# Optimization experiments

Measured on AMD Instinct MI355X. Metric: run time of the kernel, lower is better.

Reference implementation:

```python
import jax, jax.numpy as jnp
import numpy as np

B, S, D, L, V = 2, 1024, 1024, 8, 32000
EPS = 1e-8


def rmsnorm(x, w):
    return x * jax.lax.rsqrt(jnp.mean(x * x, axis=-1, keepdims=True) + EPS) * w


def lerp_scan(v, a):
    # h_t = (1 - a_t) * h_{t-1} + a_t * v_t over time axis=1 (h_0 = 0)
    A = 1.0 - a
    Bv = a * v
    def comb(l, r):
        return (l[0] * r[0], l[1] * r[0] + r[1])
    _, h = jax.lax.associative_scan(comb, (A, Bv), axis=1)
    return h


def mrt_layer(x, kw, cw, cb, w1, b1, w2, b2, nw):
    res = x @ kw                                   # [B,S,2D]
    theta, alpha = jnp.split(res, 2, axis=-1)
    h = lerp_scan(jnp.tanh(theta) * jnp.pi, jax.nn.sigmoid(alpha))  # [B,S,D]
    # causal depthwise conv, kernel 3, manual left pad of 2
    hc = jnp.pad(h.transpose(0, 2, 1), ((0, 0), (0, 0), (2, 0)))    # [B,D,S+2]
    hb = jax.lax.conv_general_dilated(
        hc, cw, window_strides=(1,), padding='VALID',
        dimension_numbers=('NCH', 'OIH', 'NCH'), feature_group_count=D)
    hb = (hb + cb[None, :, None]).transpose(0, 2, 1)                # [B,S,D]
    z = h + hb
    hf = jax.nn.silu(z @ w1 + b1) @ w2 + b2
    return rmsnorm(hf, nw)


def setup_inputs() -> dict:
    key = jax.random.key(0)
    ks = jax.random.split(key, 10)
    s = 0.02
    return {
        'input_ids': jax.random.randint(ks[0], (B, S), 0, V),
        'embedding': jax.random.normal(ks[1], (V, D), dtype=jnp.float32) * 0.002,
        'pos_emb': jax.random.normal(ks[2], (1, 1024, D), dtype=jnp.float32) * 0.002,
        'keygen_w': jax.random.normal(ks[3], (L, D, 2 * D), dtype=jnp.float32) * s,
        'conv_w': jax.random.normal(ks[4], (L, D, 1, 3), dtype=jnp.float32) * s,
        'conv_b': jnp.zeros((L, D), dtype=jnp.float32),
        'mlp_w1': jax.random.normal(ks[5], (L, D, 2 * D), dtype=jnp.float32) * s,
        'mlp_b1': jnp.zeros((L, 2 * D), dtype=jnp.float32),
        'mlp_w2': jax.random.normal(ks[6], (L, 2 * D, D), dtype=jnp.float32) * s,
        'mlp_b2': jnp.zeros((L, D), dtype=jnp.float32),
        'norm_w': jnp.ones((L, D), dtype=jnp.float32),
        'plastic': jnp.zeros((4, D, D), dtype=jnp.float32),
        'final_norm_w': jnp.ones((D,), dtype=jnp.float32),
    }


def reference(input_ids, embedding, pos_emb, keygen_w, conv_w, conv_b,
              mlp_w1, mlp_b1, mlp_w2, mlp_b2, norm_w, plastic, final_norm_w):
    seq = input_ids.shape[1]
    x = embedding[input_ids] + pos_emb[:, :seq, :]
    x = x / jnp.maximum(jnp.linalg.norm(x, axis=-1, keepdims=True), 1e-12)  # F.normalize
    for i in range(L):
        delta = mrt_layer(x, keygen_w[i], conv_w[i], conv_b[i],
                          mlp_w1[i], mlp_b1[i], mlp_w2[i], mlp_b2[i], norm_w[i])
        if i >= L - 4:
            x = x + delta + delta @ plastic[i - (L - 4)]
        else:
            x = x + delta
    x = rmsnorm(x, final_norm_w)
    # eval mode: dropout is identity
    x = x * jax.lax.rsqrt(jnp.mean(x * x, axis=-1, keepdims=True) + 1e-8) * 0.8
    logits = x @ embedding.T                       # tied lm_head
    std = jnp.std(logits, axis=-1, keepdims=True, ddof=1)  # torch.std unbiased
    logits = logits / jnp.maximum(std, 1.0)
    return jnp.clip(logits, -10.0, 10.0)
```

## Files before the change

kernel.cpp:

```cpp
#include <hip/hip_runtime.h>


using short8 = __attribute__((ext_vector_type(8))) short;
using half8  = __attribute__((ext_vector_type(8))) _Float16;
using f32x4  = __attribute__((ext_vector_type(4))) float;

#define DEVI __device__ __forceinline__

DEVI float sigm(float x) { return 1.0f / (1.0f + expf(-x)); }

DEVI float block_sum256(float v) {
  #pragma unroll
  for (int o = 32; o > 0; o >>= 1) v += __shfl_down(v, o, 64);
  __shared__ float sm[4];
  if ((threadIdx.x & 63) == 0) sm[threadIdx.x >> 6] = v;
  __syncthreads();
  float t = sm[0] + sm[1] + sm[2] + sm[3];
  __syncthreads();
  return t;
}

DEVI void gload16(const void* g, void* l) {
  __builtin_amdgcn_global_load_lds(
      (const __attribute__((address_space(1))) unsigned*)g,
      (__attribute__((address_space(3))) unsigned*)l, 16, 0, 0);
}

template<int EPI, int KSPLIT>
__global__ __launch_bounds__(256, 2) void gemm9(
    const _Float16* __restrict__ A, const _Float16* __restrict__ B,
    int M, int N, int K,
    float* __restrict__ outF, _Float16* __restrict__ outH,
    const float* __restrict__ bias,
    float* __restrict__ psum, float* __restrict__ psq, int halfN)
{
  __shared__ __align__(16) unsigned short lds[2][2][128 * 64];
  const int tid  = threadIdx.x;
  const int lane = tid & 63, wid = tid >> 6;
  const int wr = wid >> 1, wc = wid & 1;
  const int myr = lane & 15;
  const int kq  = lane >> 4;

  const int nwg  = gridDim.x;
  const int flat = blockIdx.x;
  const int swz  = (flat & 7) * (nwg >> 3) + (flat >> 3);
  const int ks   = (KSPLIT > 1) ? (swz % KSPLIT) : 0;
  const int tile = (KSPLIT > 1) ? (swz / KSPLIT) : swz;
  const int MT   = M >> 7;
  const int m0   = (tile % MT) * 128;
  const int nt   = tile / MT;
  const int n0   = nt * 128;
  const int Kc   = K / KSPLIT;
  const int kbase = ks * Kc;
  const int NT   = Kc / 64;

  auto stage = [&](int b, int k0) {
    #pragma unroll
    for (int q = 0; q < 4; ++q) {
      const int row  = q * 32 + wid * 8 + (lane >> 3);
      const int scol = ((lane & 7) ^ (row & 7)) << 3;
      const int lb   = (q * 32 + wid * 8) * 64;
      gload16(A + (size_t)(m0 + row) * K + k0 + scol, &lds[b][0][lb]);
      gload16(B + (size_t)(n0 + row) * K + k0 + scol, &lds[b][1][lb]);
    }
  };

  f32x4 acc[4][4] = {};

  stage(0, kbase);
  stage(1, kbase + 64);
  for (int t = 0; t < NT; ++t) {
    const int b = t & 1;
    if (t + 1 < NT) { asm volatile("s_waitcnt vmcnt(8)" ::: "memory"); }
    else            { asm volatile("s_waitcnt vmcnt(0)" ::: "memory"); }
    __builtin_amdgcn_s_barrier();
    asm volatile("" ::: "memory");

    #pragma unroll
    for (int kk = 0; kk < 2; ++kk) {
      short8 af[4], bf[4];
      #pragma unroll
      for (int i = 0; i < 4; ++i) {
        const int ra = wr * 64 + i * 16 + myr;
        af[i] = *(const short8*)&lds[b][0][ra * 64 + (((kk * 4 + kq) ^ (ra & 7)) << 3)];
      }
      #pragma unroll
      for (int j = 0; j < 4; ++j) {
        const int rb = wc * 64 + j * 16 + myr;
        bf[j] = *(const short8*)&lds[b][1][rb * 64 + (((kk * 4 + kq) ^ (rb & 7)) << 3)];
      }
      asm volatile("s_waitcnt lgkmcnt(0)" ::: "memory");
      if (kk == 1) {
        __builtin_amdgcn_s_barrier();
        asm volatile("" ::: "memory");
        if (t + 2 < NT) stage(b, kbase + (t + 2) * 64);
      }
      __builtin_amdgcn_sched_barrier(0);
      __builtin_amdgcn_s_setprio(1);
      #pragma unroll
      for (int i = 0; i < 4; ++i)
        #pragma unroll
        for (int j = 0; j < 4; ++j)
          acc[i][j] = __builtin_amdgcn_mfma_f32_16x16x32_f16(
              __builtin_bit_cast(half8, af[i]), __builtin_bit_cast(half8, bf[j]),
              acc[i][j], 0, 0, 0);
      __builtin_amdgcn_s_setprio(0);
    }
  }

  const size_t MN = (size_t)M * N;
  #pragma unroll
  for (int i = 0; i < 4; ++i) {
    const int rbase = m0 + wr * 64 + i * 16 + (kq << 2);
    #pragma unroll
    for (int j = 0; j < 4; ++j) {
      const int col = n0 + wc * 64 + j * 16 + myr;
      if constexpr (EPI == 1) {
        f32x4 v;
        #pragma unroll
        for (int r = 0; r < 4; ++r) {
          float c = acc[i][j][r];
          v[r] = (col < halfN) ? (tanhf(c) * 3.14159265358979323846f) : sigm(c);
        }
        *(f32x4*)&outF[(size_t)col * M + rbase] = v;
      } else {
        #pragma unroll
        for (int r = 0; r < 4; ++r) {
          float c = acc[i][j][r];
          const size_t idx = (size_t)(rbase + r) * N + col;
          if constexpr (EPI == 0) {
            outF[idx] = c;
          } else if constexpr (EPI == 2) {
            c += bias[col];
            outH[idx] = (_Float16)(c * sigm(c));
          } else if constexpr (EPI == 4) {
            float xn = outF[idx] + c;
            outF[idx] = xn;
            outH[idx] = (_Float16)xn;
          } else if constexpr (EPI == 5) {
            outF[(size_t)ks * MN + idx] = c;
          }
        }
      }
    }
  }

  if constexpr (EPI == 0) {
    const int PW = N >> 6;
    const int pcol = nt * 2 + wc;
    #pragma unroll
    for (int i = 0; i < 4; ++i)
      #pragma unroll
      for (int r = 0; r < 4; ++r) {
        float s = 0.f, ss = 0.f;
        #pragma unroll
        for (int j = 0; j < 4; ++j) {
          float v = acc[i][j][r];
          s += v; ss += v * v;
        }
        #pragma unroll
        for (int mk = 1; mk < 16; mk <<= 1) {
          s  += __shfl_xor(s,  mk, 64);
          ss += __shfl_xor(ss, mk, 64);
        }
        if (myr == i * 4 + r) {
          const int row = m0 + wr * 64 + i * 16 + kq * 4 + r;
          psum[(size_t)row * PW + pcol] = s;
          psq [(size_t)row * PW + pcol] = ss;
        }
      }
  }
}

__global__ __launch_bounds__(256) void scanconv(
    const float* __restrict__ vaT, const float* __restrict__ cw,
    const float* __restrict__ cb, _Float16* __restrict__ z16,
    int S, int D, int M)
{
  const int dl = threadIdx.x & 7;
  const int c  = threadIdx.x >> 3;
  const int ch = blockIdx.x * 8 + dl;
  const int b = ch >> 10, d = ch & 1023;
  const float* vrow = vaT + (size_t)d * M + b * S;
  const float* arow = vaT + (size_t)(D + d) * M + b * S;
  const int s0 = c * 32;

  f32x4 vr[8], ar[8];
  float A = 1.f, Bv = 0.f, Apm = 1.f, Bpm = 0.f;
  #pragma unroll
  for (int t = 0; t < 8; ++t) {
    vr[t] = *(const f32x4*)&vrow[s0 + t * 4];
    ar[t] = *(const f32x4*)&arow[s0 + t * 4];
    #pragma unroll
    for (int r = 0; r < 4; ++r) {
      if (t * 4 + r == 31) { Apm = A; Bpm = Bv; }
      float na = 1.f - ar[t][r];
      A *= na;
      Bv = Bv * na + ar[t][r] * vr[t][r];
    }
  }
  __shared__ float Asm[32][9], Bsm[32][9], Aps[32][9], Bps[32][9];
  Asm[c][dl] = A; Bsm[c][dl] = Bv; Aps[c][dl] = Apm; Bps[c][dl] = Bpm;
  __syncthreads();
  if (threadIdx.x < 8) {
    float run = 0.f;
    for (int cc = 0; cc < 32; ++cc) {
      float A_ = Asm[cc][dl], B_ = Bsm[cc][dl];
      Bsm[cc][dl] = run;
      run = A_ * run + B_;
    }
  }
  __syncthreads();
  float hm1 = Bsm[c][dl];
  float hm2 = (c == 0) ? 0.f
            : (Aps[c - 1][dl] * Bsm[c - 1][dl] + Bps[c - 1][dl]);

  const float w0 = cw[d * 3 + 0], w1 = cw[d * 3 + 1], w2 = cw[d * 3 + 2];
  const float bc = cb[d];
  #pragma unroll
  for (int t = 0; t < 8; ++t) {
    #pragma unroll
    for (int r = 0; r < 4; ++r) {
      float h = hm1 + ar[t][r] * (vr[t][r] - hm1);
      float z = h + bc + w0 * hm2 + w1 * hm1 + w2 * h;
      z16[(size_t)(b * S + s0 + t * 4 + r) * D + d] = (_Float16)z;
      hm2 = hm1; hm1 = h;
    }
  }
}

__global__ __launch_bounds__(256) void rms_fuse(
    const float* __restrict__ p, const float* __restrict__ bias,
    const float* __restrict__ nw, float* __restrict__ x,
    _Float16* __restrict__ o16, int D, int mode, size_t MN)
{
  const size_t base = (size_t)blockIdx.x * D;
  float vloc[4]; float ss = 0.f;
  #pragma unroll
  for (int q = 0; q < 4; ++q) {
    int d = threadIdx.x + q * 256;
    float v = p[base + d] + p[MN + base + d] + bias[d];
    vloc[q] = v; ss += v * v;
  }
  ss = block_sum256(ss);
  float r = 1.f / sqrtf(ss / D + 1e-8f);
  #pragma unroll
  for (int q = 0; q < 4; ++q) {
    int d = threadIdx.x + q * 256;
    float delta = vloc[q] * r * nw[d];
    float xn = x[base + d] + delta;
    x[base + d] = xn;
    o16[base + d] = (_Float16)(mode ? delta : xn);
  }
}

__global__ __launch_bounds__(256) void embed_norm(
    const int* __restrict__ ids, const float* __restrict__ emb,
    const float* __restrict__ pos,
    float* __restrict__ x, _Float16* __restrict__ x16, int S, int D)
{
  const int rowi = blockIdx.x;
  const int s = rowi % S;
  const int tok = ids[rowi];
  const size_t eb = (size_t)tok * D, pb = (size_t)s * D, xb = (size_t)rowi * D;
  float vloc[4]; float ss = 0.f;
  #pragma unroll
  for (int q = 0; q < 4; ++q) {
    int d = threadIdx.x + q * 256;
    float v = emb[eb + d] + pos[pb + d];
    vloc[q] = v; ss += v * v;
  }
  ss = block_sum256(ss);
  float r = 1.f / fmaxf(sqrtf(ss), 1e-12f);
  #pragma unroll
  for (int q = 0; q < 4; ++q) {
    int d = threadIdx.x + q * 256;
    float v = vloc[q] * r;
    x[xb + d] = v;
    x16[xb + d] = (_Float16)v;
  }
}

__global__ __launch_bounds__(256) void final_norm(
    const float* __restrict__ x, const float* __restrict__ w,
    _Float16* __restrict__ xf, int D)
{
  const size_t base = (size_t)blockIdx.x * D;
  float s1 = 0.f, s2 = 0.f;
  float vloc[4], wloc[4];
  #pragma unroll
  for (int q = 0; q < 4; ++q) {
    int d = threadIdx.x + q * 256;
    float v = x[base + d], ww = w[d];
    vloc[q] = v; wloc[q] = ww;
    s1 += v * v; s2 += v * ww * v * ww;
  }
  s1 = block_sum256(s1);
  s2 = block_sum256(s2);
  float r1 = 1.f / sqrtf(s1 / D + 1e-8f);
  float m2 = r1 * r1 * (s2 / D);
  float r2 = 1.f / sqrtf(m2 + 1e-8f);
  float sc = r1 * r2 * 0.8f;
  #pragma unroll
  for (int q = 0; q < 4; ++q) {
    int d = threadIdx.x + q * 256;
    xf[base + d] = (_Float16)(vloc[q] * wloc[q] * sc);
  }
}

__global__ __launch_bounds__(256) void fix_row(
    float* __restrict__ out, const float* __restrict__ psum,
    const float* __restrict__ psq, int PW, int V)
{
  const int row = blockIdx.x;
  float s = 0.f, q = 0.f;
  for (int j = threadIdx.x; j < PW; j += 256) {
    s += psum[(size_t)row * PW + j];
    q += psq [(size_t)row * PW + j];
  }
  s = block_sum256(s);
  q = block_sum256(q);
  float mean = s / V;
  float var = (q - (float)V * mean * mean) / (float)(V - 1);
  var = fmaxf(var, 0.f);
  const float sc = 1.f / fmaxf(sqrtf(var), 1.f);
  float* rowp = out + (size_t)row * V;
  for (int j = threadIdx.x * 4; j < V; j += 1024) {
    f32x4 v = *(f32x4*)&rowp[j];
    #pragma unroll
    for (int t = 0; t < 4; ++t)
      v[t] = fminf(fmaxf(v[t] * sc, -10.f), 10.f);
    *(f32x4*)&rowp[j] = v;
  }
}

__global__ void tsplit16(const float* __restrict__ W, _Float16* __restrict__ WT,
                         int K, int N)
{
  __shared__ float t[32][33];
  const size_t bo = (size_t)blockIdx.z * K * N;
  const int tx = threadIdx.x, ty = threadIdx.y;
  #pragma unroll
  for (int i = 0; i < 32; i += 8) {
    int kk = blockIdx.y * 32 + ty + i;
    int nn = blockIdx.x * 32 + tx;
    t[ty + i][tx] = W[bo + (size_t)kk * N + nn];
  }
  __syncthreads();
  #pragma unroll
  for (int i = 0; i < 32; i += 8) {
    int nn = blockIdx.x * 32 + ty + i;
    int kk = blockIdx.y * 32 + tx;
    WT[bo + (size_t)nn * K + kk] = (_Float16)t[tx][ty + i];
  }
}

__global__ void cvt_f16(const float* __restrict__ in, _Float16* __restrict__ o, size_t n)
{
  for (size_t i = (size_t)blockIdx.x * 256 + threadIdx.x; i < n;
       i += (size_t)gridDim.x * 256)
    o[i] = (_Float16)in[i];
}

extern "C" void kernel_launch(void* const* d_in, const int* in_sizes, int n_in,
                              void* d_out, int out_size, void* d_ws, size_t ws_size,
                              hipStream_t stream)
{
  (void)in_sizes; (void)n_in; (void)out_size; (void)ws_size;
  const int*   ids = (const int*)  d_in[0];
  const float* emb = (const float*)d_in[1];
  const float* pos = (const float*)d_in[2];
  const float* kw  = (const float*)d_in[3];
  const float* cw  = (const float*)d_in[4];
  const float* cb  = (const float*)d_in[5];
  const float* w1  = (const float*)d_in[6];
  const float* b1  = (const float*)d_in[7];
  const float* w2  = (const float*)d_in[8];
  const float* b2  = (const float*)d_in[9];
  const float* nw  = (const float*)d_in[10];
  const float* pl  = (const float*)d_in[11];
  const float* fnw = (const float*)d_in[12];
  float* out = (float*)d_out;

  constexpr int B = 2, S = 1024, D = 1024, L = 8, V = 32000;
  constexpr int M = B * S;
  const size_t MN = (size_t)M * D;

  size_t off = 0;
  auto alloc = [&](size_t bytes) {
    char* p = (char*)d_ws + off;
    off += (bytes + 255) & ~(size_t)255;
    return (void*)p;
  };
  _Float16* kwT  = (_Float16*)alloc((size_t)L * 2 * D * D * 2);
  _Float16* w1T  = (_Float16*)alloc((size_t)L * 2 * D * D * 2);
  _Float16* w2T  = (_Float16*)alloc((size_t)L * 2 * D * D * 2);
  _Float16* plT  = (_Float16*)alloc((size_t)4 * D * D * 2);
  _Float16* emb16 = (_Float16*)alloc((size_t)V * D * 2);
  float* x    = (float*)alloc(MN * 4);
  _Float16* x16 = (_Float16*)alloc(MN * 2);
  float* vaT  = (float*)alloc((size_t)M * 2 * D * 4);
  float* pbig = (float*)alloc(2 * MN * 4);
  _Float16* z16 = (_Float16*)alloc(MN * 2);
  _Float16* u16 = (_Float16*)alloc((size_t)M * 2 * D * 2);
  _Float16* d16 = (_Float16*)alloc(MN * 2);
  _Float16* xf16 = (_Float16*)alloc(MN * 2);

  const int PW = V >> 6;
  float* psum = vaT;
  float* psq  = vaT + (size_t)M * PW;

  {
    dim3 tb(32, 8);
    tsplit16<<<dim3(2 * D / 32, D / 32, L), tb, 0, stream>>>(kw, kwT, D, 2 * D);
    tsplit16<<<dim3(2 * D / 32, D / 32, L), tb, 0, stream>>>(w1, w1T, D, 2 * D);
    tsplit16<<<dim3(D / 32, 2 * D / 32, L), tb, 0, stream>>>(w2, w2T, 2 * D, D);
    tsplit16<<<dim3(D / 32, D / 32, 4),     tb, 0, stream>>>(pl, plT, D, D);
    cvt_f16<<<4096, 256, 0, stream>>>(emb, emb16, (size_t)V * D);
  }

  embed_norm<<<M, 256, 0, stream>>>(ids, emb, pos, x, x16, S, D);

  for (int i = 0; i < L; ++i) {
    const _Float16* kwi = kwT + (size_t)i * 2 * D * D;
    const _Float16* w1i = w1T + (size_t)i * 2 * D * D;
    const _Float16* w2i = w2T + (size_t)i * 2 * D * D;

    gemm9<1, 1><<<(M / 128) * (2 * D / 128), 256, 0, stream>>>(
        x16, kwi, M, 2 * D, D, vaT, nullptr, nullptr, nullptr, nullptr, D);

    scanconv<<<B * D / 8, 256, 0, stream>>>(
        vaT, cw + (size_t)i * D * 3, cb + (size_t)i * D, z16, S, D, M);

    gemm9<2, 1><<<(M / 128) * (2 * D / 128), 256, 0, stream>>>(
        z16, w1i, M, 2 * D, D, nullptr, u16, b1 + (size_t)i * 2 * D,
        nullptr, nullptr, 0);

    gemm9<5, 2><<<(M / 128) * (D / 128) * 2, 256, 0, stream>>>(
        u16, w2i, M, D, 2 * D, pbig, nullptr, nullptr, nullptr, nullptr, 0);

    const int mode = (i >= L - 4) ? 1 : 0;
    rms_fuse<<<M, 256, 0, stream>>>(pbig, b2 + (size_t)i * D, nw + (size_t)i * D,
                                    x, mode ? d16 : x16, D, mode, MN);
    if (mode) {
      const _Float16* pli = plT + (size_t)(i - 4) * D * D;
      gemm9<4, 1><<<(M / 128) * (D / 128), 256, 0, stream>>>(
          d16, pli, M, D, D, x, x16, nullptr, nullptr, nullptr, 0);
    }
  }

  final_norm<<<M, 256, 0, stream>>>(x, fnw, xf16, D);

  gemm9<0, 1><<<(M / 128) * (V / 128), 256, 0, stream>>>(
      xf16, emb16, M, V, D, out, nullptr, nullptr, psum, psq, 0);

  fix_row<<<M, 256, 0, stream>>>(out, psum, psq, PW, V);
}
```

Measured before the change: 1.172 ms.

## Use 256x256 tile, 8-wave pipelined GEMM for the LM-head logits projection

Adds a new gemm10h kernel with 256x256 output tiles, 512 threads and a double-buffered, half-tile staged LDS pipeline that interleaves global loads with MFMA quarters, plus a raised wave priority during MFMA. It replaces the 128x128 gemm9<0> for the V=32000 logits GEMM, keeping the fused row partial-sum and sum-of-squares epilogue. The larger tile is meant to cut global and LDS traffic per FLOP, but it needs 128 KB of LDS and more registers, which may limit occupancy. V/256 = 125 tiles, so N divides evenly.

```diff
diff --git a/kernel.cpp b/kernel.cpp
--- a/kernel.cpp
+++ b/kernel.cpp
@@ -26,13 +26,164 @@
       (__attribute__((address_space(3))) unsigned*)l, 16, 0, 0);
 }
 
+__global__ __launch_bounds__(512, 2) void gemm10h(
+    const _Float16* __restrict__ A, const _Float16* __restrict__ B,
+    int M, int N, int K,
+    float* __restrict__ outF, float* __restrict__ psum, float* __restrict__ psq)
+{
+  __shared__ __align__(16) unsigned short lds[2][2][2][128 * 64];
+  const int tid  = threadIdx.x;
+  const int lane = tid & 63, wid = tid >> 6;
+  const int wr = wid >> 2, wc = wid & 3;
+  const int myr = lane & 15;
+  const int kq  = lane >> 4;
+
+  const int nwg  = gridDim.x;
+  const int flat = blockIdx.x;
+  const int swz  = (flat & 7) * (nwg >> 3) + (flat >> 3);
+  const int MT   = M >> 8;
+  const int m0   = (swz % MT) * 256;
+  const int nt   = swz / MT;
+  const int n0   = nt * 256;
+  const int NT   = K / 64;
+  const int NITER = NT / 2;
+
+  auto stageH = [&](int d, int arr, int h, int tileK, const _Float16* P,
+                    int rowbase) {
+    const int k0 = tileK * 64;
+    #pragma unroll
+    for (int q = 0; q < 2; ++q) {
+      const int r = q * 64 + wid * 8 + (lane >> 3);
+      const int scol = ((lane & 7) ^ (r & 7)) << 3;
+      gload16(P + (size_t)(rowbase + h * 128 + r) * K + k0 + scol,
+              &lds[d][arr][h][(q * 64 + wid * 8) * 64]);
+    }
+  };
+
+  f32x4 acc[8][4] = {};
+  short8 afr[2][4], bf0[2][2], bf1[2][2];
+
+  auto readA = [&](int d, int qi) {
+    #pragma unroll
+    for (int kk = 0; kk < 2; ++kk)
+      #pragma unroll
+      for (int i = 0; i < 4; ++i) {
+        const int ra = qi * 64 + i * 16 + myr;
+        afr[kk][i] = *(const short8*)
+            &lds[d][0][wr][ra * 64 + (((kk * 4 + kq) ^ (ra & 7)) << 3)];
+      }
+  };
+  auto readB = [&](int d, int qj, short8 bf[2][2]) {
+    #pragma unroll
+    for (int kk = 0; kk < 2; ++kk)
+      #pragma unroll
+      for (int j = 0; j < 2; ++j) {
+        const int rn = wc * 64 + qj * 32 + j * 16 + myr;
+        const int h = rn >> 7, rb = rn & 127;
+        bf[kk][j] = *(const short8*)
+            &lds[d][1][h][rb * 64 + (((kk * 4 + kq) ^ (rb & 7)) << 3)];
+      }
+  };
+  auto mfma16 = [&](int qi, int qj, short8 bf[2][2]) {
+    asm volatile("s_waitcnt lgkmcnt(0)" ::: "memory");
+    __builtin_amdgcn_sched_barrier(0);
+    __builtin_amdgcn_s_setprio(1);
+    #pragma unroll
+    for (int kk = 0; kk < 2; ++kk)
+      #pragma unroll
+      for (int i = 0; i < 4; ++i)
+        #pragma unroll
+        for (int j = 0; j < 2; ++j)
+          acc[qi * 4 + i][qj * 2 + j] = __builtin_amdgcn_mfma_f32_16x16x32_f16(
+              __builtin_bit_cast(half8, afr[kk][i]),
+              __builtin_bit_cast(half8, bf[kk][j]),
+              acc[qi * 4 + i][qj * 2 + j], 0, 0, 0);
+    __builtin_amdgcn_s_setprio(0);
+  };
+  auto bar = [&] { __builtin_amdgcn_s_barrier(); asm volatile("" ::: "memory"); };
+
+  stageH(0, 0, 0, 0, A, m0); stageH(0, 0, 1, 0, A, m0);
+  stageH(0, 1, 0, 0, B, n0); stageH(0, 1, 1, 0, B, n0);
+  stageH(1, 1, 0, 1, B, n0); stageH(1, 1, 1, 1, B, n0);
+  asm volatile("s_waitcnt vmcnt(4)" ::: "memory");
+  bar();
+
+  for (int it = 0; it < NITER; ++it) {
+    const int Tp = 2 * it + 1, Tn = 2 * it + 2, Tn1 = 2 * it + 3;
+    readA(0, 0); readB(0, 0, bf0);
+    stageH(1, 0, 0, Tp, A, m0);
+    bar(); mfma16(0, 0, bf0); bar();
+    readB(0, 1, bf1);
+    stageH(1, 0, 1, Tp, A, m0);
+    bar(); mfma16(0, 1, bf1); bar();
+    readA(0, 1);
+    if (Tn < NT) stageH(0, 1, 0, Tn, B, n0);
+    bar(); mfma16(1, 1, bf1); bar();
+    if (Tn < NT) stageH(0, 1, 1, Tn, B, n0);
+    bar(); mfma16(1, 0, bf0);
+    if (it + 1 < NITER) { asm volatile("s_waitcnt vmcnt(4)" ::: "memory"); }
+    else                { asm volatile("s_waitcnt vmcnt(0)" ::: "memory"); }
+    bar();
+    readA(1, 0); readB(1, 0, bf0);
+    if (Tn < NT) stageH(0, 0, 0, Tn, A, m0);
+    bar(); mfma16(0, 0, bf0); bar();
+    readB(1, 1, bf1);
+    if (Tn < NT) stageH(0, 0, 1, Tn, A, m0);
+    bar(); mfma16(0, 1, bf1); bar();
+    readA(1, 1);
+    if (Tn1 < NT) stageH(1, 1, 0, Tn1, B, n0);
+    bar(); mfma16(1, 1, bf1); bar();
+    if (Tn1 < NT) stageH(1, 1, 1, Tn1, B, n0);
+    bar(); mfma16(1, 0, bf0);
+    if (it + 1 < NITER) {
+      asm volatile("s_waitcnt vmcnt(4)" ::: "memory");
+      bar();
+    }
+  }
+
+  #pragma unroll
+  for (int i8 = 0; i8 < 8; ++i8) {
+    const int rbase = m0 + wr * 128 + i8 * 16 + (kq << 2);
+    #pragma unroll
+    for (int j4 = 0; j4 < 4; ++j4) {
+      const int col = n0 + wc * 64 + j4 * 16 + myr;
+      #pragma unroll
+      for (int r = 0; r < 4; ++r)
+        outF[(size_t)(rbase + r) * N + col] = acc[i8][j4][r];
+    }
+  }
+
+  const int PW = N >> 6;
+  const int pcol = (n0 >> 6) + wc;
+  #pragma unroll
+  for (int i8 = 0; i8 < 8; ++i8)
+    #pragma unroll
+    for (int r = 0; r < 4; ++r) {
+      float s = 0.f, ss = 0.f;
+      #pragma unroll
+      for (int j4 = 0; j4 < 4; ++j4) {
+        float v = acc[i8][j4][r];
+        s += v; ss += v * v;
+      }
+      #pragma unroll
+      for (int mk = 1; mk < 16; mk <<= 1) {
+        s  += __shfl_xor(s,  mk, 64);
+        ss += __shfl_xor(ss, mk, 64);
+      }
+      if (myr == ((i8 * 4 + r) & 15)) {
+        const int row = m0 + wr * 128 + i8 * 16 + kq * 4 + r;
+        psum[(size_t)row * PW + pcol] = s;
+        psq [(size_t)row * PW + pcol] = ss;
+      }
+    }
+}
+
 template<int EPI, int KSPLIT>
 __global__ __launch_bounds__(256, 2) void gemm9(
     const _Float16* __restrict__ A, const _Float16* __restrict__ B,
     int M, int N, int K,
     float* __restrict__ outF, _Float16* __restrict__ outH,
-    const float* __restrict__ bias,
-    float* __restrict__ psum, float* __restrict__ psq, int halfN)
+    const float* __restrict__ bias, int halfN)
 {
   __shared__ __align__(16) unsigned short lds[2][2][128 * 64];
   const int tid  = threadIdx.x;
@@ -48,8 +199,7 @@
   const int tile = (KSPLIT > 1) ? (swz / KSPLIT) : swz;
   const int MT   = M >> 7;
   const int m0   = (tile % MT) * 128;
-  const int nt   = tile / MT;
-  const int n0   = nt * 128;
+  const int n0   = (tile / MT) * 128;
   const int Kc   = K / KSPLIT;
   const int kbase = ks * Kc;
   const int NT   = Kc / 64;
@@ -128,9 +278,7 @@
         for (int r = 0; r < 4; ++r) {
           float c = acc[i][j][r];
           const size_t idx = (size_t)(rbase + r) * N + col;
-          if constexpr (EPI == 0) {
-            outF[idx] = c;
-          } else if constexpr (EPI == 2) {
+          if constexpr (EPI == 2) {
             c += bias[col];
             outH[idx] = (_Float16)(c * sigm(c));
           } else if constexpr (EPI == 4) {
@@ -143,32 +291,6 @@
         }
       }
     }
-  }
-
-  if constexpr (EPI == 0) {
-    const int PW = N >> 6;
-    const int pcol = nt * 2 + wc;
-    #pragma unroll
-    for (int i = 0; i < 4; ++i)
-      #pragma unroll
-      for (int r = 0; r < 4; ++r) {
-        float s = 0.f, ss = 0.f;
-        #pragma unroll
-        for (int j = 0; j < 4; ++j) {
-          float v = acc[i][j][r];
-          s += v; ss += v * v;
-        }
-        #pragma unroll
-        for (int mk = 1; mk < 16; mk <<= 1) {
-          s  += __shfl_xor(s,  mk, 64);
-          ss += __shfl_xor(ss, mk, 64);
-        }
-        if (myr == i * 4 + r) {
-          const int row = m0 + wr * 64 + i * 16 + kq * 4 + r;
-          psum[(size_t)row * PW + pcol] = s;
-          psq [(size_t)row * PW + pcol] = ss;
-        }
-      }
   }
 }
 
@@ -427,17 +549,16 @@
     const _Float16* w2i = w2T + (size_t)i * 2 * D * D;
 
     gemm9<1, 1><<<(M / 128) * (2 * D / 128), 256, 0, stream>>>(
-        x16, kwi, M, 2 * D, D, vaT, nullptr, nullptr, nullptr, nullptr, D);
+        x16, kwi, M, 2 * D, D, vaT, nullptr, nullptr, D);
 
     scanconv<<<B * D / 8, 256, 0, stream>>>(
         vaT, cw + (size_t)i * D * 3, cb + (size_t)i * D, z16, S, D, M);
 
     gemm9<2, 1><<<(M / 128) * (2 * D / 128), 256, 0, stream>>>(
-        z16, w1i, M, 2 * D, D, nullptr, u16, b1 + (size_t)i * 2 * D,
-        nullptr, nullptr, 0);
+        z16, w1i, M, 2 * D, D, nullptr, u16, b1 + (size_t)i * 2 * D, 0);
 
     gemm9<5, 2><<<(M / 128) * (D / 128) * 2, 256, 0, stream>>>(
-        u16, w2i, M, D, 2 * D, pbig, nullptr, nullptr, nullptr, nullptr, 0);
+        u16, w2i, M, D, 2 * D, pbig, nullptr, nullptr, 0);
 
     const int mode = (i >= L - 4) ? 1 : 0;
     rms_fuse<<<M, 256, 0, stream>>>(pbig, b2 + (size_t)i * D, nw + (size_t)i * D,
@@ -445,14 +566,14 @@
     if (mode) {
       const _Float16* pli = plT + (size_t)(i - 4) * D * D;
       gemm9<4, 1><<<(M / 128) * (D / 128), 256, 0, stream>>>(
-          d16, pli, M, D, D, x, x16, nullptr, nullptr, nullptr, 0);
+          d16, pli, M, D, D, x, x16, nullptr, 0);
     }
   }
 
   final_norm<<<M, 256, 0, stream>>>(x, fnw, xf16, D);
 
-  gemm9<0, 1><<<(M / 128) * (V / 128), 256, 0, stream>>>(
-      xf16, emb16, M, V, D, out, nullptr, nullptr, psum, psq, 0);
+  gemm10h<<<(M / 256) * (V / 256), 512, 0, stream>>>(
+      xf16, emb16, M, V, D, out, psum, psq);
 
   fix_row<<<M, 256, 0, stream>>>(out, psum, psq, PW, V);
 }
```

Result: faster. 1.135 ms (-3.2%).
